# Performance work log

Hardware: AMD Instinct MI355X
Metric: run time of the kernel (lower is better)

Reference implementation:

```python
import jax, jax.numpy as jnp
import numpy as np

D_MODEL = 2048
EXPAND = 2
D_INNER = D_MODEL * EXPAND            # 4096
HEAD_DIM = 64
NHEADS = D_INNER // HEAD_DIM          # 64
D_STATE = 128
NGROUPS = 1
D_CONV = 4
CHUNK = 256
CONV_DIM = D_INNER + 2 * NGROUPS * D_STATE      # 4352
D_IN_PROJ = 2 * D_INNER + 2 * NGROUPS * D_STATE + NHEADS  # 8512
EPS = 1e-5


def segsum(x):
    # x: [..., T] -> [..., T, T] lower-triangular segment sums (incl. diagonal)
    T = x.shape[-1]
    xc = jnp.cumsum(x, axis=-1)
    diff = xc[..., :, None] - xc[..., None, :]
    mask = jnp.tril(jnp.ones((T, T), dtype=bool))
    return jnp.where(mask, diff, -jnp.inf)


def causal_conv1d(x, w, b):
    # x: [B,L,C]  depthwise causal conv, kernel K; w: [C,K], b: [C]
    K = w.shape[1]
    L = x.shape[1]
    xp = jnp.pad(x, ((0, 0), (K - 1, 0), (0, 0)))
    y = b[None, None, :]
    for k in range(K):
        y = y + xp[:, k:k + L, :] * w[None, None, :, k]
    return jax.nn.silu(y)


def ssd_chunked(x, dt, A, B, C, Dskip):
    # x:[b,l,h,p] dt:[b,l,h] A:[h] B,C:[b,l,g,n] Dskip:[h]
    b, l, h, p = x.shape
    g, n = B.shape[2], B.shape[3]
    c = l // CHUNK
    xc = x.reshape(b, c, CHUNK, h, p)
    dtc = dt.reshape(b, c, CHUNK, h)
    Bh = jnp.repeat(B.reshape(b, c, CHUNK, g, n), h // g, axis=3)  # [b,c,s,h,n]
    Ch = jnp.repeat(C.reshape(b, c, CHUNK, g, n), h // g, axis=3)
    dA = dtc * A[None, None, None, :]            # [b,c,s,h]
    dAc = jnp.moveaxis(dA, 3, 1)                 # [b,h,c,s]
    A_cumsum = jnp.cumsum(dAc, axis=-1)          # [b,h,c,s]
    Lmat = jnp.exp(segsum(dAc))                  # [b,h,c,s,s]
    # intra-chunk (diagonal blocks)
    Y_diag = jnp.einsum('bclhn,bcshn,bhcls,bcsh,bcshp->bclhp', Ch, Bh, Lmat, dtc, xc)
    # per-chunk final states
    decay_states = jnp.exp(A_cumsum[..., -1:] - A_cumsum)   # [b,h,c,s]
    states = jnp.einsum('bclhn,bhcl,bclh,bclhp->bchpn', Bh, decay_states, dtc, xc)
    states = jnp.concatenate([jnp.zeros_like(states[:, :1]), states], axis=1)  # [b,c+1,h,p,n]
    # inter-chunk recurrence
    chunk_sums = jnp.pad(A_cumsum[..., -1], ((0, 0), (0, 0), (1, 0)))  # [b,h,c+1]
    decay_chunk = jnp.exp(segsum(chunk_sums))    # [b,h,c+1,c+1]
    new_states = jnp.einsum('bhzc,bchpn->bzhpn', decay_chunk, states)
    states_prev = new_states[:, :-1]             # state entering each chunk
    state_decay_out = jnp.exp(A_cumsum)          # [b,h,c,s]
    Y_off = jnp.einsum('bclhn,bchpn,bhcl->bclhp', Ch, states_prev, state_decay_out)
    Y = (Y_diag + Y_off).reshape(b, l, h, p) + x * Dskip[None, None, :, None]
    return Y


def gated_rmsnorm(y, z, w):
    # norm_before_gate=False: rmsnorm(y * silu(z)) * w, grouped (g=NGROUPS)
    x = y * jax.nn.silu(z)
    gs = D_INNER // NGROUPS
    xg = x.reshape(x.shape[:-1] + (NGROUPS, gs))
    var = jnp.mean(xg * xg, axis=-1, keepdims=True)
    xg = xg * jax.lax.rsqrt(var + EPS)
    return xg.reshape(x.shape) * w[None, None, :]


def setup_inputs() -> dict:
    key = jax.random.key(0)
    ks = jax.random.split(key, 9)
    B, L = 2, 2048
    return {
        'hidden_states': jax.random.normal(ks[0], (B, L, D_MODEL), jnp.float32),
        'W_in': jax.random.normal(ks[1], (D_MODEL, D_IN_PROJ), jnp.float32) * 0.02,
        'conv_w': jax.random.normal(ks[2], (CONV_DIM, D_CONV), jnp.float32) * 0.2,
        'conv_b': jax.random.normal(ks[3], (CONV_DIM,), jnp.float32) * 0.02,
        'A': -jnp.exp(jax.random.normal(ks[4], (NHEADS,), jnp.float32) * 0.5),
        'D': jax.random.normal(ks[5], (NHEADS,), jnp.float32) * 0.5,
        'dt_bias': jax.random.normal(ks[6], (NHEADS,), jnp.float32) * 0.5,
        'norm_w': jnp.ones((D_INNER,), jnp.float32) + jax.random.normal(ks[7], (D_INNER,), jnp.float32) * 0.02,
        'W_out': jax.random.normal(ks[8], (D_INNER, D_MODEL), jnp.float32) * 0.02,
    }


def reference(hidden_states, W_in, conv_w, conv_b, A, D, dt_bias, norm_w, W_out):
    b, l, _ = hidden_states.shape
    zxbcdt = hidden_states @ W_in  # [b,l,d_in_proj]
    z = zxbcdt[..., :D_INNER]
    xbc = zxbcdt[..., D_INNER:D_INNER + CONV_DIM]
    dt = zxbcdt[..., D_INNER + CONV_DIM:]
    xbc = causal_conv1d(xbc, conv_w, conv_b)
    x = xbc[..., :D_INNER].reshape(b, l, NHEADS, HEAD_DIM)
    Bs = xbc[..., D_INNER:D_INNER + NGROUPS * D_STATE].reshape(b, l, NGROUPS, D_STATE)
    Cs = xbc[..., D_INNER + NGROUPS * D_STATE:].reshape(b, l, NGROUPS, D_STATE)
    dt = jax.nn.softplus(dt + dt_bias[None, None, :])
    y = ssd_chunked(x, dt, A, Bs, Cs, D).reshape(b, l, D_INNER)
    y = gated_rmsnorm(y, z, norm_w)
    return y @ W_out
```

## Files before the change

### kernel.cpp

```cpp
#include <hip/hip_runtime.h>
#include <hip/hip_bf16.h>
#include <math.h>

#define D_MODEL   2048
#define D_INNER   4096
#define NHEADS    64
#define HEAD_DIM  64
#define D_STATE   128
#define CHUNK     256
#define CONV_DIM  (D_INNER + 2*D_STATE)
#define D_IN_PROJ (2*D_INNER + 2*D_STATE + NHEADS)
#define LD_ZX     8704
#define DT_OFF    (2*D_INNER + 2*D_STATE)
#define BATCH     2
#define SEQ       2048
#define NCHUNK    (SEQ/CHUNK)
#define EPS_RMS   1e-5f

typedef unsigned short u16;
typedef __attribute__((ext_vector_type(8))) unsigned short u16x8;
typedef __attribute__((ext_vector_type(4))) unsigned short u16x4;
typedef __attribute__((ext_vector_type(8))) short bf16x8;
typedef __attribute__((ext_vector_type(4))) float f32x4;

__device__ __forceinline__ float us2f(u16 u){
    union { unsigned int i; float f; } c; c.i = ((unsigned int)u) << 16; return c.f;
}
__device__ __forceinline__ u16 f2us(float f){
    union { float f; unsigned int i; } c; c.f = f;
    unsigned int r = c.i + 0x7FFFu + ((c.i >> 16) & 1u);
    return (u16)(r >> 16);
}
__device__ __forceinline__ float siluf(float x){ return x / (1.f + expf(-x)); }

__device__ __forceinline__ void gload_lds16(const void* g, void* l) {
    __builtin_amdgcn_global_load_lds((const __attribute__((address_space(1))) void*)g,
                                     (__attribute__((address_space(3))) void*)l, 16, 0, 0);
}

#define VMCNT(n) asm volatile("s_waitcnt vmcnt(" #n ")" ::: "memory")

__device__ __forceinline__ void stage_half(const u16* __restrict__ g, size_t ldk,
                                           u16* ldsbase, int w, int lane)
{
    #pragma unroll
    for (int cc = 0; cc < 2; cc++) {
        int cb = cc * 512 + w * 64;
        int ci = cb + lane;
        int sc = ci ^ ((ci >> 3) & 7);
        gload_lds16(&g[(size_t)(sc >> 3) * ldk + (sc & 7) * 8], ldsbase + cb * 8);
    }
}

__global__ __launch_bounds__(256)
void cvt_bf16(const float* __restrict__ in, u16* __restrict__ out, int n4)
{
    int i = blockIdx.x * 256 + threadIdx.x;
    if (i >= n4) return;
    float4 v = *(const float4*)&in[(size_t)i * 4];
    u16x4 o; o[0]=f2us(v.x); o[1]=f2us(v.y); o[2]=f2us(v.z); o[3]=f2us(v.w);
    *(u16x4*)&out[(size_t)i * 4] = o;
}

__global__ __launch_bounds__(256)
void add_f32(float* __restrict__ out, const float* __restrict__ tmp, int n4)
{
    int i = blockIdx.x * 256 + threadIdx.x;
    if (i >= n4) return;
    float4 a = *(const float4*)&out[(size_t)i * 4];
    float4 b = *(const float4*)&tmp[(size_t)i * 4];
    *(float4*)&out[(size_t)i * 4] = make_float4(a.x+b.x, a.y+b.y, a.z+b.z, a.w+b.w);
}

__global__ __launch_bounds__(256)
void add4_cvt_tail(const float* __restrict__ tp, u16* __restrict__ zx, int M)
{
    int idx = blockIdx.x * 256 + threadIdx.x;
    int r = idx >> 6, c8 = idx & 63;
    const size_t stride = (size_t)M * 512;
    const float* p = &tp[(size_t)r * 512 + c8 * 8];
    u16x8 o;
    #pragma unroll
    for (int e = 0; e < 8; e++) {
        float s = p[e] + p[stride + e] + p[2*stride + e] + p[3*stride + e];
        o[e] = f2us(s);
    }
    *(u16x8*)&zx[(size_t)r * LD_ZX + 8192 + c8 * 8] = o;
}

__global__ __launch_bounds__(256)
void transpose_cvt(const float* __restrict__ in, u16* __restrict__ out, int K, int N)
{
    __shared__ u16 tile[64][65];
    int k0 = blockIdx.x * 64;
    int n0 = blockIdx.y * 64;
    int t = threadIdx.x;
    #pragma unroll
    for (int q = 0; q < 16; q++) {
        int lin = q * 256 + t;
        int r = lin >> 6, c = lin & 63;
        int n = n0 + c;
        float v = (n < N) ? in[(size_t)(k0 + r) * N + n] : 0.f;
        tile[r][c] = f2us(v);
    }
    __syncthreads();
    #pragma unroll
    for (int q = 0; q < 4; q++) {
        int lin = q * 256 + t;
        int r = lin >> 4, cg = lin & 15;
        u16x4 v;
        #pragma unroll
        for (int e = 0; e < 4; e++) v[e] = tile[cg*4 + e][r];
        *(u16x4*)&out[(size_t)(n0 + r) * K + k0 + cg*4] = v;
    }
}

template<typename TC, bool KSPLIT>
__global__ __launch_bounds__(512, 1)
void gemm_8ph(const u16* __restrict__ Ag, const u16* __restrict__ Btg,
              TC* __restrict__ Cg, TC* __restrict__ Cg2,
              int M, int N, int Kext, int ldk, int ldc)
{
    __shared__ u16 smA[2][2][8192];
    __shared__ u16 smB[2][2][8192];
    const int tid = threadIdx.x;
    const int lane = tid & 63, w = tid >> 6;
    const int wm = w >> 2, wn = w & 3;
    const int lr = lane & 15, kh = lane >> 4;
    const int swz = (lr & 7) << 3;

    int orig = blockIdx.x;
    int ntile = gridDim.x;
    int kidx = 0;
    if constexpr (KSPLIT) { kidx = orig & 1; orig >>= 1; ntile >>= 1; }

    const int nbx = N >> 8;
    const int qq = ntile >> 3, r8 = ntile & 7;
    const int xcd = orig & 7, loc = orig >> 3;
    const int wgid = (xcd < r8 ? xcd*(qq+1) : r8*(qq+1) + (xcd-r8)*qq) + loc;
    const int m0 = (wgid / nbx) * 256;
    const int n0 = (wgid % nbx) * 256;

    if constexpr (KSPLIT) {
        Ag  += (size_t)kidx * Kext;
        Btg += (size_t)kidx * Kext;
        if (kidx) Cg = Cg2;
    }
    const int NT = Kext >> 6;

    f32x4 acc[8][4];
    #pragma unroll
    for (int i = 0; i < 8; i++)
        #pragma unroll
        for (int j = 0; j < 4; j++) acc[i][j] = (f32x4){0.f,0.f,0.f,0.f};

    stage_half(&Ag [(size_t)(m0      ) * ldk      ], ldk, &smA[0][0][0], w, lane);
    stage_half(&Ag [(size_t)(m0 + 128) * ldk      ], ldk, &smA[0][1][0], w, lane);
    stage_half(&Btg[(size_t)(n0      ) * ldk      ], ldk, &smB[0][0][0], w, lane);
    stage_half(&Btg[(size_t)(n0 + 128) * ldk      ], ldk, &smB[0][1][0], w, lane);
    stage_half(&Ag [(size_t)(m0      ) * ldk + 64 ], ldk, &smA[1][0][0], w, lane);
    stage_half(&Btg[(size_t)(n0      ) * ldk + 64 ], ldk, &smB[1][0][0], w, lane);
    stage_half(&Btg[(size_t)(n0 + 128) * ldk + 64 ], ldk, &smB[1][1][0], w, lane);
    VMCNT(6);
    __builtin_amdgcn_s_barrier();

    for (int t = 0; t < NT; ++t) {
        const int d = t & 1;
        const u16* As = &smA[d][wm][0];
        const u16* Bs = &smB[d][wn >> 1][0];
        const int rb = (wn & 1) * 64;

        bf16x8 aF[4][2], bLo[2][2], bHi[2][2];

        #pragma unroll
        for (int i = 0; i < 4; i++)
            #pragma unroll
            for (int ks = 0; ks < 2; ks++)
                aF[i][ks] = *(const bf16x8*)&As[(i*16 + lr)*64 + ((ks*32 + kh*8) ^ swz)];
        #pragma unroll
        for (int j = 0; j < 2; j++)
            #pragma unroll
            for (int ks = 0; ks < 2; ks++)
                bLo[j][ks] = *(const bf16x8*)&Bs[(rb + j*16 + lr)*64 + ((ks*32 + kh*8) ^ swz)];
        if (t + 1 < NT)
            stage_half(&Ag[(size_t)(m0 + 128) * ldk + (t+1)*64], ldk, &smA[d^1][1][0], w, lane);
        __builtin_amdgcn_s_barrier();
        __builtin_amdgcn_s_setprio(1);
        #pragma unroll
        for (int i = 0; i < 4; i++)
            #pragma unroll
            for (int j = 0; j < 2; j++)
                #pragma unroll
                for (int ks = 0; ks < 2; ks++)
                    acc[i][j] = __builtin_amdgcn_mfma_f32_16x16x32_bf16(aF[i][ks], bLo[j][ks], acc[i][j], 0, 0, 0);
        __builtin_amdgcn_s_setprio(0);
        __builtin_amdgcn_s_barrier();

        #pragma unroll
        for (int j = 0; j < 2; j++)
            #pragma unroll
            for (int ks = 0; ks < 2; ks++)
                bHi[j][ks] = *(const bf16x8*)&Bs[(rb + (2+j)*16 + lr)*64 + ((ks*32 + kh*8) ^ swz)];
        __builtin_amdgcn_s_barrier();
        __builtin_amdgcn_s_setprio(1);
        #pragma unroll
        for (int i = 0; i < 4; i++)
            #pragma unroll
            for (int j = 0; j < 2; j++)
                #pragma unroll
                for (int ks = 0; ks < 2; ks++)
                    acc[i][2+j] = __builtin_amdgcn_mfma_f32_16x16x32_bf16(aF[i][ks], bHi[j][ks], acc[i][2+j], 0, 0, 0);
        __builtin_amdgcn_s_setprio(0);
        __builtin_amdgcn_s_barrier();

        #pragma unroll
        for (int i = 0; i < 4; i++)
            #pragma unroll
            for (int ks = 0; ks < 2; ks++)
                aF[i][ks] = *(const bf16x8*)&As[(64 + i*16 + lr)*64 + ((ks*32 + kh*8) ^ swz)];
        if (t + 2 < NT)
            stage_half(&Btg[(size_t)(n0) * ldk + (t+2)*64], ldk, &smB[d][0][0], w, lane);
        __builtin_amdgcn_s_barrier();
        __builtin_amdgcn_s_setprio(1);
        #pragma unroll
        for (int i = 0; i < 4; i++)
            #pragma unroll
            for (int j = 0; j < 2; j++)
                #pragma unroll
                for (int ks = 0; ks < 2; ks++)
                    acc[4+i][j] = __builtin_amdgcn_mfma_f32_16x16x32_bf16(aF[i][ks], bLo[j][ks], acc[4+i][j], 0, 0, 0);
        __builtin_amdgcn_s_setprio(0);
        __builtin_amdgcn_s_barrier();

        if (t + 2 < NT) {
            stage_half(&Btg[(size_t)(n0 + 128) * ldk + (t+2)*64], ldk, &smB[d][1][0], w, lane);
            stage_half(&Ag [(size_t)(m0      ) * ldk + (t+2)*64], ldk, &smA[d][0][0], w, lane);
        }
        __builtin_amdgcn_s_barrier();
        __builtin_amdgcn_s_setprio(1);
        #pragma unroll
        for (int i = 0; i < 4; i++)
            #pragma unroll
            for (int j = 0; j < 2; j++)
                #pragma unroll
                for (int ks = 0; ks < 2; ks++)
                    acc[4+i][2+j] = __builtin_amdgcn_mfma_f32_16x16x32_bf16(aF[i][ks], bHi[j][ks], acc[4+i][2+j], 0, 0, 0);
        __builtin_amdgcn_s_setprio(0);
        if (t < NT - 2)       { VMCNT(6); }
        else if (t == NT - 2) { VMCNT(0); }
        __builtin_amdgcn_s_barrier();
    }

    #pragma unroll
    for (int mf = 0; mf < 8; mf++) {
        #pragma unroll
        for (int nf = 0; nf < 4; nf++) {
            int r = m0 + wm*128 + mf*16 + kh*4;
            int cidx = n0 + wn*64 + nf*16 + lr;
            #pragma unroll
            for (int q = 0; q < 4; q++) {
                if constexpr (sizeof(TC) == 4) Cg[(size_t)(r+q)*ldc + cidx] = acc[mf][nf][q];
                else                           Cg[(size_t)(r+q)*ldc + cidx] = f2us(acc[mf][nf][q]);
            }
        }
    }
}

__global__ __launch_bounds__(256)
void gemm_tail_ks4(const u16* __restrict__ A, const u16* __restrict__ Bt,
                   float* __restrict__ Cp, int M, int ldk)
{
    __shared__ u16 Asm[128][32];
    __shared__ u16 Bsm[128][32];
    const int t = threadIdx.x;
    const int lane = t & 63, w = t >> 6;
    const int wr = w >> 1, wc = w & 1;
    const int lr = lane & 15, kh = lane >> 4;

    const int bid = blockIdx.x;
    const int kidx = bid & 3, tile = bid >> 2;
    const int m0 = (tile >> 2) * 128;
    const int n0 = (tile & 3) * 128;

    const u16* Ak = A  + kidx * 512;
    const u16* Bk = Bt + kidx * 512;
    float* C = Cp + (size_t)kidx * M * 512;

    f32x4 acc[4][4];
    #pragma unroll
    for (int i = 0; i < 4; i++)
        #pragma unroll
        for (int j = 0; j < 4; j++) acc[i][j] = (f32x4){0.f,0.f,0.f,0.f};

    for (int k0 = 0; k0 < 512; k0 += 32) {
        #pragma unroll
        for (int i = 0; i < 2; i++) {
            int cb = i * 256 + w * 64;
            int chunk = cb + lane;
            int row = chunk >> 2, kb = chunk & 3;
            gload_lds16(&Ak[(size_t)(m0 + row) * ldk + k0 + kb * 8], &Asm[0][0] + cb * 8);
            gload_lds16(&Bk[(size_t)(n0 + row) * ldk + k0 + kb * 8], &Bsm[0][0] + cb * 8);
        }
        __syncthreads();
        bf16x8 af[4], bf[4];
        #pragma unroll
        for (int i = 0; i < 4; i++)
            af[i] = *(const bf16x8*)&Asm[wr*64 + i*16 + lr][kh*8];
        #pragma unroll
        for (int j = 0; j < 4; j++)
            bf[j] = *(const bf16x8*)&Bsm[wc*64 + j*16 + lr][kh*8];
        #pragma unroll
        for (int i = 0; i < 4; i++)
            #pragma unroll
            for (int j = 0; j < 4; j++)
                acc[i][j] = __builtin_amdgcn_mfma_f32_16x16x32_bf16(af[i], bf[j], acc[i][j], 0, 0, 0);
        __syncthreads();
    }
    #pragma unroll
    for (int i = 0; i < 4; i++) {
        #pragma unroll
        for (int j = 0; j < 4; j++) {
            int r = m0 + wr*64 + i*16 + kh*4;
            int cidx = n0 + wc*64 + j*16 + lr;
            #pragma unroll
            for (int q = 0; q < 4; q++)
                C[(size_t)(r+q)*512 + cidx] = acc[i][j][q];
        }
    }
}

__global__ __launch_bounds__(256)
void conv_silu(const u16* __restrict__ zx, const float* __restrict__ cw,
               const float* __restrict__ cb, u16* __restrict__ xconv,
               u16* __restrict__ Bbuf, u16* __restrict__ Cbuf)
{
    int idx = blockIdx.x * 256 + threadIdx.x;
    int cg = idx % (CONV_DIM / 8);
    int r  = idx / (CONV_DIM / 8);
    int c0 = cg * 8;
    int l  = r & (SEQ - 1);

    float y[8];
    {
        float4 b0 = *(const float4*)&cb[c0];
        float4 b1 = *(const float4*)&cb[c0 + 4];
        y[0]=b0.x; y[1]=b0.y; y[2]=b0.z; y[3]=b0.w;
        y[4]=b1.x; y[5]=b1.y; y[6]=b1.z; y[7]=b1.w;
    }
    float cwf[8][4];
    #pragma unroll
    for (int e = 0; e < 8; e++) {
        float4 v = *(const float4*)&cw[(c0 + e) * 4];
        cwf[e][0]=v.x; cwf[e][1]=v.y; cwf[e][2]=v.z; cwf[e][3]=v.w;
    }
    #pragma unroll
    for (int k = 0; k < 4; k++) {
        if (l + k - 3 >= 0) {
            u16x8 v = *(const u16x8*)&zx[(size_t)(r + k - 3) * LD_ZX + D_INNER + c0];
            #pragma unroll
            for (int e = 0; e < 8; e++) y[e] += us2f(v[e]) * cwf[e][k];
        }
    }
    u16x8 o;
    #pragma unroll
    for (int e = 0; e < 8; e++) {
        float s = y[e] / (1.f + expf(-y[e]));
        o[e] = f2us(s);
    }
    if (c0 < D_INNER)                *(u16x8*)&xconv[(size_t)r * D_INNER + c0] = o;
    else if (c0 < D_INNER + D_STATE) *(u16x8*)&Bbuf[(size_t)r * D_STATE + (c0 - D_INNER)] = o;
    else                             *(u16x8*)&Cbuf[(size_t)r * D_STATE + (c0 - D_INNER - D_STATE)] = o;
}

__global__ __launch_bounds__(256)
void dt_acs(const u16* __restrict__ zx, const float* __restrict__ Aparam,
            const float* __restrict__ dt_bias, float* __restrict__ dtT,
            float* __restrict__ Acs)
{
    __shared__ float sb[CHUNK];
    int blk = blockIdx.x;
    int c = blk & 7, h = (blk >> 3) & 63, b = blk >> 9;
    int t = threadIdx.x;
    int lg = c * CHUNK + t;
    int row = b * SEQ + lg;
    float x = us2f(zx[(size_t)row * LD_ZX + DT_OFF + h]) + dt_bias[h];
    float dt = (x > 20.f) ? x : log1pf(expf(x));
    float v = dt * Aparam[h];
    sb[t] = v; __syncthreads();
    #pragma unroll
    for (int off = 1; off < 256; off <<= 1) {
        float add = (t >= off) ? sb[t - off] : 0.f;
        __syncthreads();
        v += add; sb[t] = v;
        __syncthreads();
    }
    int o = (b * NHEADS + h) * SEQ + lg;
    dtT[o] = dt;
    Acs[o] = v;
}

__global__ __launch_bounds__(256)
void chunk_states_mfma(const u16* __restrict__ xconv, const u16* __restrict__ Bbuf,
                       const float* __restrict__ dtT, const float* __restrict__ Acs,
                       u16* __restrict__ states)
{
    __shared__ u16 Btsh[128][72];
    __shared__ u16 xtsh[64][72];
    __shared__ float acs_sh[CHUNK];
    __shared__ float dt_sh[CHUNK];

    const int blk = blockIdx.x;
    const int h = blk & 63, c = (blk >> 6) & 7, b = blk >> 9;
    const int t = threadIdx.x;
    const int lane = t & 63, w = t >> 6;
    const int wr = w >> 1, wc = w & 1;
    const int lr = lane & 15, kh = lane >> 4;
    const int bh = b * NHEADS + h;
    const size_t rowbase = (size_t)(b * SEQ + c * CHUNK);

    acs_sh[t] = Acs[(size_t)bh * SEQ + c * CHUNK + t];
    dt_sh[t]  = dtT[(size_t)bh * SEQ + c * CHUNK + t];
    __syncthreads();
    const float acs_last = acs_sh[CHUNK - 1];

    f32x4 acc[4][2];
    #pragma unroll
    for (int j = 0; j < 4; j++)
        #pragma unroll
        for (int i = 0; i < 2; i++) acc[j][i] = (f32x4){0.f,0.f,0.f,0.f};

    for (int lt = 0; lt < 4; lt++) {
        __syncthreads();
        const int s = t & 63;
        const int sg = lt * 64 + s;
        const float wgt = dt_sh[sg] * expf(acs_last - acs_sh[sg]);
        {
            int ng = (t >> 6) * 32;
            const u16* src = &Bbuf[(rowbase + sg) * D_STATE + ng];
            #pragma unroll
            for (int q = 0; q < 4; q++) {
                u16x8 v = *(const u16x8*)&src[q * 8];
                #pragma unroll
                for (int e = 0; e < 8; e++)
                    Btsh[ng + q*8 + e][s] = v[e];
            }
        }
        {
            int pg = (t >> 6) * 16;
            const u16* src = &xconv[(rowbase + sg) * D_INNER + h * HEAD_DIM + pg];
            u16x8 v0 = *(const u16x8*)&src[0];
            u16x8 v1 = *(const u16x8*)&src[8];
            #pragma unroll
            for (int e = 0; e < 8; e++) {
                xtsh[pg + e][s]     = f2us(us2f(v0[e]) * wgt);
                xtsh[pg + 8 + e][s] = f2us(us2f(v1[e]) * wgt);
            }
        }
        __syncthreads();
        #pragma unroll
        for (int kk = 0; kk < 2; kk++) {
            bf16x8 xf[2], bf[4];
            #pragma unroll
            for (int i = 0; i < 2; i++)
                xf[i] = *(const bf16x8*)&xtsh[wr*32 + i*16 + lr][kk*32 + kh*8];
            #pragma unroll
            for (int j = 0; j < 4; j++)
                bf[j] = *(const bf16x8*)&Btsh[wc*64 + j*16 + lr][kk*32 + kh*8];
            #pragma unroll
            for (int j = 0; j < 4; j++)
                #pragma unroll
                for (int i = 0; i < 2; i++)
                    acc[j][i] = __builtin_amdgcn_mfma_f32_16x16x32_bf16(bf[j], xf[i], acc[j][i], 0, 0, 0);
        }
    }
    size_t base = ((size_t)((b*NCHUNK + c)*NHEADS + h)) * (HEAD_DIM * D_STATE);
    #pragma unroll
    for (int j = 0; j < 4; j++) {
        #pragma unroll
        for (int i = 0; i < 2; i++) {
            int p = wr*32 + i*16 + lr;
            int n = wc*64 + j*16 + kh*4;
            u16x4 o;
            #pragma unroll
            for (int q = 0; q < 4; q++) o[q] = f2us(acc[j][i][q]);
            *(u16x4*)&states[base + (size_t)p * D_STATE + n] = o;
        }
    }
}

__global__ __launch_bounds__(256)
void state_recurrence(u16* __restrict__ states, const float* __restrict__ Acs)
{
    int idx = blockIdx.x * 256 + threadIdx.x;
    int n8 = idx & 15;
    int p  = (idx >> 4) & 63;
    int bh = idx >> 10;
    int b = bh >> 6, h = bh & 63;
    float E[8];
    #pragma unroll
    for (int e = 0; e < 8; e++) E[e] = 0.f;
    for (int c = 0; c < NCHUNK; c++) {
        size_t off = ((size_t)((b*NCHUNK + c)*NHEADS + h)) * 8192 + (size_t)p * 128 + n8 * 8;
        u16x8 sv = *(const u16x8*)&states[off];
        u16x8 ev;
        #pragma unroll
        for (int e = 0; e < 8; e++) ev[e] = f2us(E[e]);
        *(u16x8*)&states[off] = ev;
        float g = expf(Acs[(size_t)(b*NHEADS + h) * SEQ + c*CHUNK + 255]);
        #pragma unroll
        for (int e = 0; e < 8; e++) E[e] = g * E[e] + us2f(sv[e]);
    }
}

__global__ __launch_bounds__(256, 1)
void chunk_output_mfma(const u16* __restrict__ xconv, const u16* __restrict__ Bbuf,
                       const u16* __restrict__ Cbuf, const float* __restrict__ dtT,
                       const float* __restrict__ Acs, const u16* __restrict__ states,
                       const float* __restrict__ Dparam, u16* __restrict__ Y)
{
    __shared__ u16 Bsm[64][136];
    __shared__ u16 xt[64][72];
    __shared__ u16 Pt[4][64][72];
    __shared__ float acs_sh[CHUNK];
    __shared__ float dt_sh[CHUNK];

    const int blk = blockIdx.x;
    const int h = blk & 63, c = (blk >> 6) & 7, b = blk >> 9;
    const int t = threadIdx.x;
    const int lane = t & 63, w = t >> 6;
    const int lr = lane & 15, kh = lane >> 4;
    const int bh = b * NHEADS + h;
    const size_t rowbase = (size_t)(b * SEQ + c * CHUNK);

    acs_sh[t] = Acs[(size_t)bh * SEQ + c * CHUNK + t];
    dt_sh[t]  = dtT[(size_t)bh * SEQ + c * CHUNK + t];

    bf16x8 af[4][4];
    #pragma unroll
    for (int i = 0; i < 4; i++)
        #pragma unroll
        for (int kk = 0; kk < 4; kk++)
            af[i][kk] = *(const bf16x8*)&Cbuf[(rowbase + w*64 + i*16 + lr) * D_STATE + kk*32 + kh*8];

    __syncthreads();
    float acs_l[4];
    #pragma unroll
    for (int i = 0; i < 4; i++) acs_l[i] = acs_sh[w*64 + i*16 + lr];

    f32x4 yacc[4][4];
    #pragma unroll
    for (int j = 0; j < 4; j++)
        #pragma unroll
        for (int i = 0; i < 4; i++) yacc[j][i] = (f32x4){0.f,0.f,0.f,0.f};

    for (int st = 0; st < 4; st++) {
        __syncthreads();
        {
            int sr = t >> 2, cg = (t & 3) * 32;
            const u16* src = &Bbuf[(rowbase + st*64 + sr) * D_STATE + cg];
            #pragma unroll
            for (int q = 0; q < 4; q++)
                *(u16x8*)&Bsm[sr][cg + q*8] = *(const u16x8*)&src[q*8];
        }
        {
            int s = t & 63, pg = t >> 6;
            const u16* src = &xconv[(rowbase + st*64 + s) * D_INNER + h*HEAD_DIM + pg*16];
            u16x8 v0 = *(const u16x8*)&src[0];
            u16x8 v1 = *(const u16x8*)&src[8];
            #pragma unroll
            for (int q = 0; q < 8; q++) { xt[pg*16 + q][s] = v0[q]; xt[pg*16 + 8 + q][s] = v1[q]; }
        }
        __syncthreads();
        if (st > w) continue;

        f32x4 sacc[4][4];
        #pragma unroll
        for (int js = 0; js < 4; js++)
            #pragma unroll
            for (int i = 0; i < 4; i++) sacc[js][i] = (f32x4){0.f,0.f,0.f,0.f};
        #pragma unroll
        for (int kk = 0; kk < 4; kk++) {
            bf16x8 bA[4];
            #pragma unroll
            for (int js = 0; js < 4; js++)
                bA[js] = *(const bf16x8*)&Bsm[js*16 + lr][kk*32 + kh*8];
            #pragma unroll
            for (int js = 0; js < 4; js++)
                #pragma unroll
                for (int i = 0; i < 4; i++)
                    sacc[js][i] = __builtin_amdgcn_mfma_f32_16x16x32_bf16(bA[js], af[i][kk], sacc[js][i], 0, 0, 0);
        }
        #pragma unroll
        for (int js = 0; js < 4; js++) {
            int sg0 = st*64 + js*16 + kh*4;
            float as[4], ds[4];
            #pragma unroll
            for (int q = 0; q < 4; q++) { as[q] = acs_sh[sg0 + q]; ds[q] = dt_sh[sg0 + q]; }
            #pragma unroll
            for (int i = 0; i < 4; i++) {
                int lg = w*64 + i*16 + lr;
                u16x4 pv;
                #pragma unroll
                for (int q = 0; q < 4; q++) {
                    float fac = (sg0 + q <= lg) ? expf(fminf(acs_l[i] - as[q], 0.f)) * ds[q] : 0.f;
                    pv[q] = f2us(sacc[js][i][q] * fac);
                }
                *(u16x4*)&Pt[w][i*16 + lr][js*16 + kh*4] = pv;
            }
        }
        #pragma unroll
        for (int kk2 = 0; kk2 < 2; kk2++) {
            bf16x8 xA[4], pB[4];
            #pragma unroll
            for (int j = 0; j < 4; j++)
                xA[j] = *(const bf16x8*)&xt[j*16 + lr][kk2*32 + kh*8];
            #pragma unroll
            for (int i = 0; i < 4; i++)
                pB[i] = *(const bf16x8*)&Pt[w][i*16 + lr][kk2*32 + kh*8];
            #pragma unroll
            for (int j = 0; j < 4; j++)
                #pragma unroll
                for (int i = 0; i < 4; i++)
                    yacc[j][i] = __builtin_amdgcn_mfma_f32_16x16x32_bf16(xA[j], pB[i], yacc[j][i], 0, 0, 0);
        }
    }

    __syncthreads();
    {
        int p = t >> 2, ng = (t & 3) * 32;
        const u16* src = &states[((size_t)((b*NCHUNK + c)*NHEADS + h)) * 8192 + (size_t)p * 128 + ng];
        #pragma unroll
        for (int q = 0; q < 4; q++)
            *(u16x8*)&Bsm[p][ng + q*8] = *(const u16x8*)&src[q*8];
    }
    __syncthreads();
    {
        float el[4];
        #pragma unroll
        for (int i = 0; i < 4; i++) el[i] = expf(acs_l[i]);
        #pragma unroll
        for (int kk = 0; kk < 4; kk++) {
            bf16x8 pvA[4];
            #pragma unroll
            for (int j = 0; j < 4; j++)
                pvA[j] = *(const bf16x8*)&Bsm[j*16 + lr][kk*32 + kh*8];
            #pragma unroll
            for (int i = 0; i < 4; i++) {
                bf16x8 ae;
                #pragma unroll
                for (int e = 0; e < 8; e++)
                    ae[e] = (short)f2us(us2f((u16)af[i][kk][e]) * el[i]);
                #pragma unroll
                for (int j = 0; j < 4; j++)
                    yacc[j][i] = __builtin_amdgcn_mfma_f32_16x16x32_bf16(pvA[j], ae, yacc[j][i], 0, 0, 0);
            }
        }
    }

    float Dh = Dparam[h];
    #pragma unroll
    for (int i = 0; i < 4; i++) {
        #pragma unroll
        for (int j = 0; j < 4; j++) {
            size_t o = (rowbase + w*64 + i*16 + lr) * D_INNER + h*HEAD_DIM + j*16 + kh*4;
            u16x4 xv = *(const u16x4*)&xconv[o];
            u16x4 ov;
            #pragma unroll
            for (int q = 0; q < 4; q++)
                ov[q] = f2us(yacc[j][i][q] + Dh * us2f(xv[q]));
            *(u16x4*)&Y[o] = ov;
        }
    }
}

__global__ __launch_bounds__(256)
void gated_rmsnorm_k(u16* __restrict__ Y, const u16* __restrict__ zx,
                     const float* __restrict__ nw)
{
    __shared__ float xs[D_INNER];
    __shared__ float red[8];
    int row = blockIdx.x;
    int t = threadIdx.x;
    float ss = 0.f;
    for (int i = t*8; i < D_INNER; i += 2048) {
        u16x8 yv = *(const u16x8*)&Y[(size_t)row * D_INNER + i];
        u16x8 zv = *(const u16x8*)&zx[(size_t)row * LD_ZX + i];
        #pragma unroll
        for (int q = 0; q < 8; q++) {
            float x = us2f(yv[q]) * siluf(us2f(zv[q]));
            xs[i + q] = x;
            ss += x * x;
        }
    }
    #pragma unroll
    for (int off = 32; off > 0; off >>= 1) ss += __shfl_down(ss, off);
    int wid = t >> 6, lane = t & 63;
    if (lane == 0) red[wid] = ss;
    __syncthreads();
    if (t == 0) {
        float tot = red[0] + red[1] + red[2] + red[3];
        red[0] = rsqrtf(tot / (float)D_INNER + EPS_RMS);
    }
    __syncthreads();
    float sc = red[0];
    for (int i = t*8; i < D_INNER; i += 2048) {
        u16x8 o;
        #pragma unroll
        for (int q = 0; q < 8; q++) o[q] = f2us(xs[i + q] * sc * nw[i + q]);
        *(u16x8*)&Y[(size_t)row * D_INNER + i] = o;
    }
}

__global__ void ws_fail_k(float* out, float mb){ out[threadIdx.x] = mb; }

extern "C" void kernel_launch(void* const* d_in, const int* in_sizes, int n_in,
                              void* d_out, int out_size, void* d_ws, size_t ws_size,
                              hipStream_t stream)
{
    const float* hidden  = (const float*)d_in[0];
    const float* W_in    = (const float*)d_in[1];
    const float* conv_w  = (const float*)d_in[2];
    const float* conv_b  = (const float*)d_in[3];
    const float* Aparam  = (const float*)d_in[4];
    const float* Dparam  = (const float*)d_in[5];
    const float* dt_bias = (const float*)d_in[6];
    const float* norm_w  = (const float*)d_in[7];
    const float* W_out   = (const float*)d_in[8];
    float* out = (float*)d_out;

    const int M = BATCH * SEQ;

    size_t off = 0;
    char* wsb = (char*)d_ws;
    u16*   zx     = (u16*)  (wsb + off); off += (size_t)M * LD_ZX * 2;
    u16*   xconv  = (u16*)  (wsb + off); off += (size_t)M * D_INNER * 2;
    u16*   Bbuf   = (u16*)  (wsb + off); off += (size_t)M * D_STATE * 2;
    u16*   Cbuf   = (u16*)  (wsb + off); off += (size_t)M * D_STATE * 2;
    float* dtT    = (float*)(wsb + off); off += (size_t)BATCH * NHEADS * SEQ * 4;
    float* Acs    = (float*)(wsb + off); off += (size_t)BATCH * NHEADS * SEQ * 4;
    u16*   states = (u16*)  (wsb + off); off += (size_t)BATCH * NCHUNK * NHEADS * HEAD_DIM * D_STATE * 2;
    u16*   Ybuf   = (u16*)  (wsb + off); off += (size_t)M * D_INNER * 2;
    u16*   hbf    = (u16*)  (wsb + off); off += (size_t)M * D_MODEL * 2;
    u16*   WtIn   = (u16*)  (wsb + off); off += (size_t)LD_ZX * D_MODEL * 2;
    u16*   WtOut  = (u16*)  (wsb + off); off += (size_t)D_MODEL * D_INNER * 2;
    float* tailp  = (float*)states;
    float* tmpf   = (float*)zx;

    if (off > ws_size) {
        ws_fail_k<<<1, 64, 0, stream>>>(out, (float)(ws_size >> 20));
        return;
    }

    cvt_bf16<<<(M * D_MODEL / 4 + 255) / 256, 256, 0, stream>>>(hidden, hbf, M * D_MODEL / 4);
    transpose_cvt<<<dim3(D_MODEL/64, LD_ZX/64), 256, 0, stream>>>(W_in, WtIn, D_MODEL, D_IN_PROJ);
    transpose_cvt<<<dim3(D_INNER/64, D_MODEL/64), 256, 0, stream>>>(W_out, WtOut, D_INNER, D_MODEL);

    gemm_8ph<u16, false><<<(8192/256) * (M/256), 512, 0, stream>>>(
        hbf, WtIn, zx, nullptr, M, 8192, D_MODEL, D_MODEL, LD_ZX);
    gemm_tail_ks4<<<512, 256, 0, stream>>>(hbf, WtIn + (size_t)8192 * D_MODEL, tailp, M, D_MODEL);
    add4_cvt_tail<<<(M * 512 / 8) / 256, 256, 0, stream>>>(tailp, zx, M);

    conv_silu<<<(M * CONV_DIM / 8) / 256, 256, 0, stream>>>(zx, conv_w, conv_b, xconv, Bbuf, Cbuf);
    dt_acs<<<BATCH * NHEADS * NCHUNK, 256, 0, stream>>>(zx, Aparam, dt_bias, dtT, Acs);
    chunk_states_mfma<<<BATCH * NCHUNK * NHEADS, 256, 0, stream>>>(xconv, Bbuf, dtT, Acs, states);
    state_recurrence<<<(BATCH * NHEADS * 64 * 16) / 256, 256, 0, stream>>>(states, Acs);
    chunk_output_mfma<<<BATCH * NCHUNK * NHEADS, 256, 0, stream>>>(xconv, Bbuf, Cbuf, dtT, Acs, states, Dparam, Ybuf);
    gated_rmsnorm_k<<<M, 256, 0, stream>>>(Ybuf, zx, norm_w);

    gemm_8ph<float, true><<<2 * (D_MODEL/256) * (M/256), 512, 0, stream>>>(
        Ybuf, WtOut, out, tmpf, M, D_MODEL, D_INNER/2, D_INNER, D_MODEL);
    add_f32<<<(M * D_MODEL / 4 + 255) / 256, 256, 0, stream>>>(out, tmpf, M * D_MODEL / 4);
}
```

Measured before the change: 535.3 us.

## Fuse tail split-K reduction into consumers, bf16 split-K partial, reorder inter-chunk term

Removes the add4_cvt_tail kernel: conv_silu and dt_acs now sum the four split-K fp32 partials of the tail GEMM directly, and tailp gets its own workspace region instead of aliasing states. The second split-K half of the output GEMM is stored as bf16 rather than fp32, which halves that temporary's traffic but reduces the precision of the partial sum. In chunk_output, the inter-chunk state contribution is computed first and scaled by exp(Acs) after the MFMAs, which drops the per-element rescale of C and one LDS reload phase. The decay factor is also split into two exponentials, clamped at 60, to reduce exp calls.

```diff
diff --git a/kernel.cpp b/kernel.cpp
--- a/kernel.cpp
+++ b/kernel.cpp
@@ -16,6 +16,8 @@
 #define SEQ       2048
 #define NCHUNK    (SEQ/CHUNK)
 #define EPS_RMS   1e-5f
+#define MROWS     4096
+#define TSTRIDE   ((size_t)MROWS * 512)
 
 typedef unsigned short u16;
 typedef __attribute__((ext_vector_type(8))) unsigned short u16x8;
@@ -63,29 +65,16 @@
 }
 
 __global__ __launch_bounds__(256)
-void add_f32(float* __restrict__ out, const float* __restrict__ tmp, int n4)
+void add_tmp_bf16(float* __restrict__ out, const u16* __restrict__ tmp, int n8)
 {
     int i = blockIdx.x * 256 + threadIdx.x;
-    if (i >= n4) return;
-    float4 a = *(const float4*)&out[(size_t)i * 4];
-    float4 b = *(const float4*)&tmp[(size_t)i * 4];
-    *(float4*)&out[(size_t)i * 4] = make_float4(a.x+b.x, a.y+b.y, a.z+b.z, a.w+b.w);
-}
-
-__global__ __launch_bounds__(256)
-void add4_cvt_tail(const float* __restrict__ tp, u16* __restrict__ zx, int M)
-{
-    int idx = blockIdx.x * 256 + threadIdx.x;
-    int r = idx >> 6, c8 = idx & 63;
-    const size_t stride = (size_t)M * 512;
-    const float* p = &tp[(size_t)r * 512 + c8 * 8];
-    u16x8 o;
-    #pragma unroll
-    for (int e = 0; e < 8; e++) {
-        float s = p[e] + p[stride + e] + p[2*stride + e] + p[3*stride + e];
-        o[e] = f2us(s);
-    }
-    *(u16x8*)&zx[(size_t)r * LD_ZX + 8192 + c8 * 8] = o;
+    if (i >= n8) return;
+    u16x8 b = *(const u16x8*)&tmp[(size_t)i * 8];
+    float* o = &out[(size_t)i * 8];
+    float4 a0 = *(const float4*)&o[0];
+    float4 a1 = *(const float4*)&o[4];
+    *(float4*)&o[0] = make_float4(a0.x+us2f(b[0]), a0.y+us2f(b[1]), a0.z+us2f(b[2]), a0.w+us2f(b[3]));
+    *(float4*)&o[4] = make_float4(a1.x+us2f(b[4]), a1.y+us2f(b[5]), a1.z+us2f(b[6]), a1.w+us2f(b[7]));
 }
 
 __global__ __launch_bounds__(256)
@@ -118,7 +107,7 @@
 template<typename TC, bool KSPLIT>
 __global__ __launch_bounds__(512, 1)
 void gemm_8ph(const u16* __restrict__ Ag, const u16* __restrict__ Btg,
-              TC* __restrict__ Cg, TC* __restrict__ Cg2,
+              TC* __restrict__ Cg, u16* __restrict__ Cg2,
               int M, int N, int Kext, int ldk, int ldc)
 {
     __shared__ u16 smA[2][2][8192];
@@ -144,7 +133,6 @@
     if constexpr (KSPLIT) {
         Ag  += (size_t)kidx * Kext;
         Btg += (size_t)kidx * Kext;
-        if (kidx) Cg = Cg2;
     }
     const int NT = Kext >> 6;
 
@@ -259,8 +247,13 @@
             int cidx = n0 + wn*64 + nf*16 + lr;
             #pragma unroll
             for (int q = 0; q < 4; q++) {
-                if constexpr (sizeof(TC) == 4) Cg[(size_t)(r+q)*ldc + cidx] = acc[mf][nf][q];
-                else                           Cg[(size_t)(r+q)*ldc + cidx] = f2us(acc[mf][nf][q]);
+                if (KSPLIT && kidx) {
+                    Cg2[(size_t)(r+q)*ldc + cidx] = f2us(acc[mf][nf][q]);
+                } else if constexpr (sizeof(TC) == 4) {
+                    Cg[(size_t)(r+q)*ldc + cidx] = acc[mf][nf][q];
+                } else {
+                    Cg[(size_t)(r+q)*ldc + cidx] = f2us(acc[mf][nf][q]);
+                }
             }
         }
     }
@@ -284,7 +277,7 @@
 
     const u16* Ak = A  + kidx * 512;
     const u16* Bk = Bt + kidx * 512;
-    float* C = Cp + (size_t)kidx * M * 512;
+    float* C = Cp + (size_t)kidx * TSTRIDE;
 
     f32x4 acc[4][4];
     #pragma unroll
@@ -330,9 +323,9 @@
 }
 
 __global__ __launch_bounds__(256)
-void conv_silu(const u16* __restrict__ zx, const float* __restrict__ cw,
-               const float* __restrict__ cb, u16* __restrict__ xconv,
-               u16* __restrict__ Bbuf, u16* __restrict__ Cbuf)
+void conv_silu(const u16* __restrict__ zx, const float* __restrict__ tailp,
+               const float* __restrict__ cw, const float* __restrict__ cb,
+               u16* __restrict__ xconv, u16* __restrict__ Bbuf, u16* __restrict__ Cbuf)
 {
     int idx = blockIdx.x * 256 + threadIdx.x;
     int cg = idx % (CONV_DIM / 8);
@@ -353,12 +346,27 @@
         float4 v = *(const float4*)&cw[(c0 + e) * 4];
         cwf[e][0]=v.x; cwf[e][1]=v.y; cwf[e][2]=v.z; cwf[e][3]=v.w;
     }
-    #pragma unroll
-    for (int k = 0; k < 4; k++) {
-        if (l + k - 3 >= 0) {
-            u16x8 v = *(const u16x8*)&zx[(size_t)(r + k - 3) * LD_ZX + D_INNER + c0];
-            #pragma unroll
-            for (int e = 0; e < 8; e++) y[e] += us2f(v[e]) * cwf[e][k];
+    if (c0 < D_INNER) {
+        #pragma unroll
+        for (int k = 0; k < 4; k++) {
+            if (l + k - 3 >= 0) {
+                u16x8 v = *(const u16x8*)&zx[(size_t)(r + k - 3) * LD_ZX + D_INNER + c0];
+                #pragma unroll
+                for (int e = 0; e < 8; e++) y[e] += us2f(v[e]) * cwf[e][k];
+            }
+        }
+    } else {
+        int tc = c0 - D_INNER;
+        #pragma unroll
+        for (int k = 0; k < 4; k++) {
+            if (l + k - 3 >= 0) {
+                const float* tb = &tailp[(size_t)(r + k - 3) * 512 + tc];
+                #pragma unroll
+                for (int e = 0; e < 8; e++) {
+                    float s = tb[e] + tb[TSTRIDE + e] + tb[2*TSTRIDE + e] + tb[3*TSTRIDE + e];
+                    y[e] += s * cwf[e][k];
+                }
+            }
         }
     }
     u16x8 o;
@@ -373,7 +381,7 @@
 }
 
 __global__ __launch_bounds__(256)
-void dt_acs(const u16* __restrict__ zx, const float* __restrict__ Aparam,
+void dt_acs(const float* __restrict__ tailp, const float* __restrict__ Aparam,
             const float* __restrict__ dt_bias, float* __restrict__ dtT,
             float* __restrict__ Acs)
 {
@@ -383,7 +391,9 @@
     int t = threadIdx.x;
     int lg = c * CHUNK + t;
     int row = b * SEQ + lg;
-    float x = us2f(zx[(size_t)row * LD_ZX + DT_OFF + h]) + dt_bias[h];
+    const float* tb = &tailp[(size_t)row * 512 + 256 + h];
+    float x = tb[0] + tb[TSTRIDE] + tb[2*TSTRIDE] + tb[3*TSTRIDE];
+    x += dt_bias[h];
     float dt = (x > 20.f) ? x : log1pf(expf(x));
     float v = dt * Aparam[h];
     sb[t] = v; __syncthreads();
@@ -542,16 +552,42 @@
         for (int kk = 0; kk < 4; kk++)
             af[i][kk] = *(const bf16x8*)&Cbuf[(rowbase + w*64 + i*16 + lr) * D_STATE + kk*32 + kh*8];
 
+    {
+        int p = t >> 2, ng = (t & 3) * 32;
+        const u16* src = &states[((size_t)((b*NCHUNK + c)*NHEADS + h)) * 8192 + (size_t)p * 128 + ng];
+        #pragma unroll
+        for (int q = 0; q < 4; q++)
+            *(u16x8*)&Bsm[p][ng + q*8] = *(const u16x8*)&src[q*8];
+    }
     __syncthreads();
-    float acs_l[4];
-    #pragma unroll
-    for (int i = 0; i < 4; i++) acs_l[i] = acs_sh[w*64 + i*16 + lr];
+    float acs_l[4], el[4];
+    #pragma unroll
+    for (int i = 0; i < 4; i++) { acs_l[i] = acs_sh[w*64 + i*16 + lr]; el[i] = expf(acs_l[i]); }
 
     f32x4 yacc[4][4];
     #pragma unroll
     for (int j = 0; j < 4; j++)
         #pragma unroll
         for (int i = 0; i < 4; i++) yacc[j][i] = (f32x4){0.f,0.f,0.f,0.f};
+    #pragma unroll
+    for (int kk = 0; kk < 4; kk++) {
+        bf16x8 pvA[4];
+        #pragma unroll
+        for (int j = 0; j < 4; j++)
+            pvA[j] = *(const bf16x8*)&Bsm[j*16 + lr][kk*32 + kh*8];
+        #pragma unroll
+        for (int j = 0; j < 4; j++)
+            #pragma unroll
+            for (int i = 0; i < 4; i++)
+                yacc[j][i] = __builtin_amdgcn_mfma_f32_16x16x32_bf16(pvA[j], af[i][kk], yacc[j][i], 0, 0, 0);
+    }
+    #pragma unroll
+    for (int j = 0; j < 4; j++)
+        #pragma unroll
+        for (int i = 0; i < 4; i++)
+            #pragma unroll
+            for (int q = 0; q < 4; q++)
+                yacc[j][i][q] *= el[i];
 
     for (int st = 0; st < 4; st++) {
         __syncthreads();
@@ -592,17 +628,21 @@
         }
         #pragma unroll
         for (int js = 0; js < 4; js++) {
-            int sg0 = st*64 + js*16 + kh*4;
-            float as[4], ds[4];
-            #pragma unroll
-            for (int q = 0; q < 4; q++) { as[q] = acs_sh[sg0 + q]; ds[q] = dt_sh[sg0 + q]; }
+            int s0 = st*64 + js*16;
+            float as0 = acs_sh[s0];
+            int sgq = s0 + kh*4;
+            float eneg[4];
+            #pragma unroll
+            for (int q = 0; q < 4; q++)
+                eneg[q] = expf(fminf(as0 - acs_sh[sgq + q], 60.f)) * dt_sh[sgq + q];
             #pragma unroll
             for (int i = 0; i < 4; i++) {
+                float eladj = expf(acs_l[i] - as0);
                 int lg = w*64 + i*16 + lr;
                 u16x4 pv;
                 #pragma unroll
                 for (int q = 0; q < 4; q++) {
-                    float fac = (sg0 + q <= lg) ? expf(fminf(acs_l[i] - as[q], 0.f)) * ds[q] : 0.f;
+                    float fac = (sgq + q <= lg) ? eladj * eneg[q] : 0.f;
                     pv[q] = f2us(sacc[js][i][q] * fac);
                 }
                 *(u16x4*)&Pt[w][i*16 + lr][js*16 + kh*4] = pv;
@@ -622,38 +662,6 @@
                 #pragma unroll
                 for (int i = 0; i < 4; i++)
                     yacc[j][i] = __builtin_amdgcn_mfma_f32_16x16x32_bf16(xA[j], pB[i], yacc[j][i], 0, 0, 0);
-        }
-    }
-
-    __syncthreads();
-    {
-        int p = t >> 2, ng = (t & 3) * 32;
-        const u16* src = &states[((size_t)((b*NCHUNK + c)*NHEADS + h)) * 8192 + (size_t)p * 128 + ng];
-        #pragma unroll
-        for (int q = 0; q < 4; q++)
-            *(u16x8*)&Bsm[p][ng + q*8] = *(const u16x8*)&src[q*8];
-    }
-    __syncthreads();
-    {
-        float el[4];
-        #pragma unroll
-        for (int i = 0; i < 4; i++) el[i] = expf(acs_l[i]);
-        #pragma unroll
-        for (int kk = 0; kk < 4; kk++) {
-            bf16x8 pvA[4];
-            #pragma unroll
-            for (int j = 0; j < 4; j++)
-                pvA[j] = *(const bf16x8*)&Bsm[j*16 + lr][kk*32 + kh*8];
-            #pragma unroll
-            for (int i = 0; i < 4; i++) {
-                bf16x8 ae;
-                #pragma unroll
-                for (int e = 0; e < 8; e++)
-                    ae[e] = (short)f2us(us2f((u16)af[i][kk][e]) * el[i]);
-                #pragma unroll
-                for (int j = 0; j < 4; j++)
-                    yacc[j][i] = __builtin_amdgcn_mfma_f32_16x16x32_bf16(pvA[j], ae, yacc[j][i], 0, 0, 0);
-            }
         }
     }
 
@@ -743,8 +751,8 @@
     u16*   hbf    = (u16*)  (wsb + off); off += (size_t)M * D_MODEL * 2;
     u16*   WtIn   = (u16*)  (wsb + off); off += (size_t)LD_ZX * D_MODEL * 2;
     u16*   WtOut  = (u16*)  (wsb + off); off += (size_t)D_MODEL * D_INNER * 2;
-    float* tailp  = (float*)states;
-    float* tmpf   = (float*)zx;
+    float* tailp  = (float*)(wsb + off); off += 4 * TSTRIDE * 4;
+    u16*   tmpf   = (u16*)zx;
 
     if (off > ws_size) {
         ws_fail_k<<<1, 64, 0, stream>>>(out, (float)(ws_size >> 20));
@@ -758,10 +766,9 @@
     gemm_8ph<u16, false><<<(8192/256) * (M/256), 512, 0, stream>>>(
         hbf, WtIn, zx, nullptr, M, 8192, D_MODEL, D_MODEL, LD_ZX);
     gemm_tail_ks4<<<512, 256, 0, stream>>>(hbf, WtIn + (size_t)8192 * D_MODEL, tailp, M, D_MODEL);
-    add4_cvt_tail<<<(M * 512 / 8) / 256, 256, 0, stream>>>(tailp, zx, M);
-
-    conv_silu<<<(M * CONV_DIM / 8) / 256, 256, 0, stream>>>(zx, conv_w, conv_b, xconv, Bbuf, Cbuf);
-    dt_acs<<<BATCH * NHEADS * NCHUNK, 256, 0, stream>>>(zx, Aparam, dt_bias, dtT, Acs);
+
+    conv_silu<<<(M * CONV_DIM / 8) / 256, 256, 0, stream>>>(zx, tailp, conv_w, conv_b, xconv, Bbuf, Cbuf);
+    dt_acs<<<BATCH * NHEADS * NCHUNK, 256, 0, stream>>>(tailp, Aparam, dt_bias, dtT, Acs);
     chunk_states_mfma<<<BATCH * NCHUNK * NHEADS, 256, 0, stream>>>(xconv, Bbuf, dtT, Acs, states);
     state_recurrence<<<(BATCH * NHEADS * 64 * 16) / 256, 256, 0, stream>>>(states, Acs);
     chunk_output_mfma<<<BATCH * NCHUNK * NHEADS, 256, 0, stream>>>(xconv, Bbuf, Cbuf, dtT, Acs, states, Dparam, Ybuf);
@@ -769,5 +776,5 @@
 
     gemm_8ph<float, true><<<2 * (D_MODEL/256) * (M/256), 512, 0, stream>>>(
         Ybuf, WtOut, out, tmpf, M, D_MODEL, D_INNER/2, D_INNER, D_MODEL);
-    add_f32<<<(M * D_MODEL / 4 + 255) / 256, 256, 0, stream>>>(out, tmpf, M * D_MODEL / 4);
-}
+    add_tmp_bf16<<<(M * D_MODEL / 8 + 255) / 256, 256, 0, stream>>>(out, tmpf, M * D_MODEL / 8);
+}
```

Measured after the change: 476.8 us. -10.9%, faster.
